# Optimization experiments

Measured on AMD Instinct MI355X. Metric: run time of the kernel, lower is better.

Reference implementation:

```python
import jax, jax.numpy as jnp
import numpy as np


def _elu(x):
    return jnp.where(x > 0, x, jnp.expm1(x))


def setup_inputs() -> dict:
    key = jax.random.key(0)
    ks = jax.random.split(key, 12)
    B, T, E, A, S, H, L = 1024, 50, 1024, 6, 200, 200, 30
    g = lambda k, shape, s=0.05: (jax.random.normal(k, shape, jnp.float32) * s)
    return {
        "action": jax.random.normal(ks[0], (B, T, A), jnp.float32),
        "embed": jax.random.normal(ks[1], (B, T, E), jnp.float32),
        "noise": jax.random.normal(ks[2], (B, T, L), jnp.float32),
        # GRUCell params (PyTorch gate order r,z,n), stored as [in, 3S]
        "W_ih": g(ks[3], (A + E, 3 * S)),
        "W_hh": g(ks[4], (S, 3 * S)),
        "b_ih": jnp.zeros((3 * S,), jnp.float32),
        "b_hh": jnp.zeros((3 * S,), jnp.float32),
        # fc_prior: Linear(S,H) -> ELU -> Linear(H, 2L)
        "Wp1": g(ks[5], (S, H)), "bp1": jnp.zeros((H,), jnp.float32),
        "Wp2": g(ks[6], (H, 2 * L)), "bp2": jnp.zeros((2 * L,), jnp.float32),
        # fc_posterior: Linear(S+E,H) -> ELU -> Linear(H, 2L)
        "Wq1": g(ks[7], (S + E, H)), "bq1": jnp.zeros((H,), jnp.float32),
        "Wq2": g(ks[8], (H, 2 * L)), "bq2": jnp.zeros((2 * L,), jnp.float32),
    }


def reference(action, embed, noise, W_ih, W_hh, b_ih, b_hh,
              Wp1, bp1, Wp2, bp2, Wq1, bq1, Wq2, bq2):
    B = action.shape[0]
    S = W_hh.shape[0]

    def gru(x, h):
        # PyTorch GRUCell: gates r, z, n
        gi = x @ W_ih + b_ih
        gh = h @ W_hh + b_hh
        i_r, i_z, i_n = jnp.split(gi, 3, -1)
        h_r, h_z, h_n = jnp.split(gh, 3, -1)
        r = jax.nn.sigmoid(i_r + h_r)
        z = jax.nn.sigmoid(i_z + h_z)
        n = jnp.tanh(i_n + r * h_n)
        return (1.0 - z) * n + z * h

    def step(deter, inp):
        a_t, e_t, eps_t = inp  # [B,A], [B,E], [B,L]
        deter = gru(jnp.concatenate([a_t, e_t], -1), deter)
        pm, ps = jnp.split(_elu(deter @ Wp1 + bp1) @ Wp2 + bp2, 2, -1)
        qm, qs = jnp.split(
            _elu(jnp.concatenate([deter, e_t], -1) @ Wq1 + bq1) @ Wq2 + bq2, 2, -1)
        ps = jax.nn.softplus(ps) + 0.1
        qs = jax.nn.softplus(qs) + 0.1
        stoch = qm + qs * eps_t  # posterior rsample
        return deter, (deter, stoch, pm, ps, qm, qs)

    deter0 = jnp.zeros((B, S), action.dtype)
    xs = (jnp.swapaxes(action, 0, 1),
          jnp.swapaxes(embed, 0, 1),
          jnp.swapaxes(noise, 0, 1))
    _, outs = jax.lax.scan(step, deter0, xs)
    # [T,B,*] -> [B,T,*]; pack (deter, stoch, prior mean/std, post mean/std)
    outs = [jnp.swapaxes(o, 0, 1) for o in outs]
    return jnp.concatenate(outs, -1)  # [B, T, S + 5L]
```

## Files before the change

### kernel.cpp

```cpp
#include <hip/hip_runtime.h>
#include <hip/hip_bf16.h>
#include <cstdint>


typedef __attribute__((ext_vector_type(8))) short   short8;
typedef __attribute__((ext_vector_type(8))) __bf16  bf16x8;
typedef __attribute__((ext_vector_type(4))) float   f32x4;

__device__ __forceinline__ float bf2f(unsigned short u) {
    unsigned int v = ((unsigned int)u) << 16;
    return __builtin_bit_cast(float, v);
}
__device__ __forceinline__ unsigned short f2bf(float f) {
    unsigned int v = __builtin_bit_cast(unsigned int, f);
    v = v + 0x7FFFu + ((v >> 16) & 1u);
    return (unsigned short)(v >> 16);
}
__device__ __forceinline__ float softplusf(float x) {
    return (x > 20.f) ? x : log1pf(__expf(x));
}
__device__ __forceinline__ void gload_lds16(const void* g, void* l) {
    __builtin_amdgcn_global_load_lds(
        (const __attribute__((address_space(1))) void*)g,
        (__attribute__((address_space(3))) void*)l, 16, 0, 0);
}

#define OFF_BPACK 81920000
#define OFF_WHH   83558400
#define OFF_WPQ1  83837952
#define OFF_WPQ2  84024320


__global__ __launch_bounds__(256) void pack_kernel(
    const float* __restrict__ W_ih, const float* __restrict__ W_hh,
    const float* __restrict__ Wp1,  const float* __restrict__ Wq1,
    const float* __restrict__ Wp2,  const float* __restrict__ Wq2,
    unsigned short* __restrict__ Bpack, unsigned short* __restrict__ Whh_p,
    unsigned short* __restrict__ Wpq1,  unsigned short* __restrict__ Wpq2)
{
    int e = blockIdx.x * 256 + threadIdx.x;
    if (e < 819200) {
        const int j = e & 7, l = (e >> 3) & 63;
        const int nt = (e >> 9) % 50, kk = e / (512 * 50);
        const int k = kk * 32 + (l >> 4) * 8 + j;
        const int c = nt * 16 + (l & 15);
        Bpack[e] = f2bf((c < 600) ? W_ih[(6 + k) * 600 + c]
                                  : Wq1[(200 + k) * 200 + (c - 600)]);
        return;
    }
    e -= 819200;
    if (e < 139776) {
        const int j = e & 7, l = (e >> 3) & 63;
        const int nt = (e >> 9) % 39, kk = e / (512 * 39);
        const int k = kk * 32 + (l >> 4) * 8 + j;
        const int g = nt / 13, st = nt % 13;
        const int c = st * 16 + (l & 15);
        Whh_p[e] = (k < 200 && c < 200) ? f2bf(W_hh[k * 600 + g * 200 + c]) : (unsigned short)0;
        return;
    }
    e -= 139776;
    if (e < 93184) {
        const int j = e & 7, l = (e >> 3) & 63;
        const int nt = (e >> 9) % 26, kk = e / (512 * 26);
        const int k = kk * 32 + (l >> 4) * 8 + j;
        unsigned short v = 0;
        if (nt < 13) { const int c = nt * 16 + (l & 15);        if (k < 200 && c < 200) v = f2bf(Wp1[k * 200 + c]); }
        else         { const int c = (nt - 13) * 16 + (l & 15); if (k < 200 && c < 200) v = f2bf(Wq1[k * 200 + c]); }
        Wpq1[e] = v;
        return;
    }
    e -= 93184;
    if (e < 28672) {
        const int j = e & 7, l = (e >> 3) & 63;
        const int nt = (e >> 9) % 8, kk = e / (512 * 8);
        const int k = kk * 32 + (l >> 4) * 8 + j;
        unsigned short v = 0;
        if (nt < 4) { const int c = nt * 16 + (l & 15);       if (k < 200 && c < 60) v = f2bf(Wp2[k * 60 + c]); }
        else        { const int c = (nt - 4) * 16 + (l & 15); if (k < 200 && c < 60) v = f2bf(Wq2[k * 60 + c]); }
        Wpq2[e] = v;
    }
}

#define K1_BYTES 26624
__global__ __launch_bounds__(256, 3) void k1_gi(
    const float* __restrict__ embed,
    const float* __restrict__ action,
    const float* __restrict__ W_ih,
    const float* __restrict__ b_ih,
    const float* __restrict__ bq1,
    const unsigned short* __restrict__ Bpack,
    unsigned short* __restrict__ GI)
{
    __shared__ char bufS[2][K1_BYTES];

    const int tid = threadIdx.x;
    const int w = tid >> 6, l = tid & 63;
    const int lo = l & 15, hi = l >> 4;

    const int g    = (blockIdx.x & 7) * 250 + (blockIdx.x >> 3);
    const int mblk = g / 5;
    const int ng   = g - mblk * 5;
    const int rb   = mblk * 128;

    const char* sp[7]; int st[7]; int dof[7];
    const int nch = (w < 2) ? 7 : 6;
#pragma unroll
    for (int i = 0; i < 7; ++i) {
        int j = w + 4 * i; if (j >= 26) j = 25;
        if (j < 10) {
            sp[i]  = (const char*)Bpack + (size_t)(ng * 10 + j) * 1024 + l * 16;
            st[i]  = 50 * 1024;
            dof[i] = j * 1024;
        } else {
            const int a = j - 10;
            sp[i]  = (const char*)embed
                   + (size_t)(rb + a * 8 + (l >> 3)) * 4096 + (l & 7) * 16;
            st[i]  = 128;
            dof[i] = 10240 + a * 1024;
        }
    }

    f32x4 acc[2][10];
#pragma unroll
    for (int m = 0; m < 2; ++m)
#pragma unroll
        for (int i = 0; i < 10; ++i) acc[m][i] = f32x4{0.f, 0.f, 0.f, 0.f};

#pragma unroll
    for (int i = 0; i < 7; ++i) if (i < nch) {
        gload_lds16(sp[i], &bufS[0][dof[i]]);
        sp[i] += st[i];
    }

    int cur = 0;
    for (int kk = 0; kk < 32; ++kk) {
        const int nxt = cur ^ 1;
        if (kk < 31) {
#pragma unroll
            for (int i = 0; i < 7; ++i) if (i < nch) {
                gload_lds16(sp[i], &bufS[nxt][dof[i]]);
                sp[i] += st[i];
            }
            if (w < 2) asm volatile("s_waitcnt vmcnt(7)" ::: "memory");
            else       asm volatile("s_waitcnt vmcnt(6)" ::: "memory");
        } else {
            asm volatile("s_waitcnt vmcnt(0)" ::: "memory");
        }
        __builtin_amdgcn_s_barrier();
        __builtin_amdgcn_sched_barrier(0);

        const float* Af = (const float*)&bufS[cur][10240];
        bf16x8 af[2];
#pragma unroll
        for (int m = 0; m < 2; ++m) {
            const int ms = w * 2 + m;
            const float* rp = Af + (ms * 16 + lo) * 32 + hi * 8;
            f32x4 v0 = *(const f32x4*)rp;
            f32x4 v1 = *(const f32x4*)(rp + 4);
            bf16x8 t;
#pragma unroll
            for (int q = 0; q < 4; ++q) { t[q] = (__bf16)v0[q]; t[4 + q] = (__bf16)v1[q]; }
            af[m] = t;
        }
#pragma unroll
        for (int i = 0; i < 10; ++i) {
            bf16x8 b = __builtin_bit_cast(bf16x8,
                *(const short8*)&bufS[cur][i * 1024 + l * 16]);
            acc[0][i] = __builtin_amdgcn_mfma_f32_16x16x32_bf16(af[0], b, acc[0][i], 0, 0, 0);
            acc[1][i] = __builtin_amdgcn_mfma_f32_16x16x32_bf16(af[1], b, acc[1][i], 0, 0, 0);
        }

        asm volatile("s_waitcnt lgkmcnt(0)" ::: "memory");
        __builtin_amdgcn_s_barrier();
        __builtin_amdgcn_sched_barrier(0);
        cur = nxt;
    }

#pragma unroll
    for (int m = 0; m < 2; ++m) {
        const int rbase = rb + (w * 2 + m) * 16 + hi * 4;
        float av[4][6];
#pragma unroll
        for (int r = 0; r < 4; ++r)
#pragma unroll
            for (int k = 0; k < 6; ++k) av[r][k] = action[(size_t)(rbase + r) * 6 + k];
#pragma unroll
        for (int i = 0; i < 10; ++i) {
            const int col = ng * 160 + i * 16 + lo;
            const float bias = (col < 600) ? b_ih[col] : bq1[col - 600];
            float wa[6];
            if (col < 600) {
#pragma unroll
                for (int k = 0; k < 6; ++k) wa[k] = W_ih[k * 600 + col];
            }
#pragma unroll
            for (int r = 0; r < 4; ++r) {
                float v = acc[m][i][r] + bias;
                if (col < 600) {
#pragma unroll
                    for (int k = 0; k < 6; ++k) v += av[r][k] * wa[k];
                }
                GI[(size_t)(rbase + r) * 800 + col] = f2bf(v);
            }
        }
    }
}

#define HSTRB 232
#define GSTR  227

__global__ __launch_bounds__(512, 2) void k2_scan(
    unsigned short* __restrict__ GI,
    const unsigned short* __restrict__ Whh_p,
    const float* __restrict__ b_hh,
    float* __restrict__ out)
{
    __shared__ unsigned short hS[16 * HSTRB];
    __shared__ float gAll[3 * 16 * GSTR];
    __shared__ __align__(16) unsigned short GIbuf[2][12288];

    const int tid = threadIdx.x;
    const int w = tid >> 6, l = tid & 63;
    const int lo = l & 15, hi = l >> 4;
    const int r0 = blockIdx.x * 16;

    for (int i = tid; i < 16 * HSTRB; i += 512) hS[i] = 0;

    const int t0 = w * 5;
    const int ntl = (w == 7) ? 4 : 5;
    bf16x8 wf[5][7];
#pragma unroll
    for (int i = 0; i < 5; ++i)
#pragma unroll
        for (int kk = 0; kk < 7; ++kk)
            if (i < ntl)
                wf[i][kk] = __builtin_bit_cast(bf16x8,
                    *(const short8*)&Whh_p[((kk * 39 + (t0 + i)) * 64 + l) * 8]);

    int gOff[5];
#pragma unroll
    for (int i = 0; i < 5; ++i) {
        int nt = t0 + i; if (nt > 38) nt = 38;
        const int g = nt / 13, st = nt - g * 13;
        gOff[i] = (g * 16 + hi * 4) * GSTR + st * 16 + lo;
    }

    const char* srcB[3];
#pragma unroll
    for (int i = 0; i < 3; ++i) {
        int j = (i * 8 + w) * 64 + l;
        int rj = j / 75; int cj = j - rj * 75;
        if (rj > 15) { rj = 15; cj = 74; }
        srcB[i] = (const char*)GI + (size_t)(r0 + rj) * 50 * 1600 + (size_t)cj * 16;
    }

    const int c = tid & 255;
    const int rh = tid >> 8;
    const bool act = (c < 200);
    float bh0 = 0.f, bh1 = 0.f, bh2 = 0.f;
    if (act) { bh0 = b_hh[c]; bh1 = b_hh[200 + c]; bh2 = b_hh[400 + c]; }
    float h_reg[8] = {0.f, 0.f, 0.f, 0.f, 0.f, 0.f, 0.f, 0.f};

    {
#pragma unroll
        for (int i = 0; i < 3; ++i)
            gload_lds16(srcB[i], &GIbuf[0][(i * 8 + w) * 512]);
    }
    asm volatile("s_waitcnt lgkmcnt(0)" ::: "memory");
    __builtin_amdgcn_s_barrier();
    __builtin_amdgcn_sched_barrier(0);

    for (int t = 0; t < 50; ++t) {
        const int tn = (t < 49) ? t + 1 : 49;
        const int bsel = (t + 1) & 1;
#pragma unroll
        for (int i = 0; i < 3; ++i)
            gload_lds16(srcB[i] + (size_t)tn * 1600, &GIbuf[bsel][(i * 8 + w) * 512]);

        bf16x8 hf[7];
#pragma unroll
        for (int kk = 0; kk < 7; ++kk)
            hf[kk] = __builtin_bit_cast(bf16x8,
                *(const short8*)&hS[lo * HSTRB + kk * 32 + hi * 8]);
        f32x4 acc[5];
#pragma unroll
        for (int i = 0; i < 5; ++i) acc[i] = f32x4{0.f, 0.f, 0.f, 0.f};
#pragma unroll
        for (int i = 0; i < 5; ++i) if (i < ntl)
#pragma unroll
            for (int kk = 0; kk < 7; ++kk)
                acc[i] = __builtin_amdgcn_mfma_f32_16x16x32_bf16(hf[kk], wf[i][kk], acc[i], 0, 0, 0);

#pragma unroll
        for (int i = 0; i < 5; ++i) if (i < ntl)
#pragma unroll
            for (int r = 0; r < 4; ++r)
                gAll[gOff[i] + r * GSTR] = acc[i][r];

        asm volatile("s_waitcnt lgkmcnt(0)" ::: "memory");
        __builtin_amdgcn_s_barrier();
        __builtin_amdgcn_sched_barrier(0);
        asm volatile("s_waitcnt vmcnt(3)" ::: "memory");
        __builtin_amdgcn_sched_barrier(0);

        if (act) {
            const unsigned short* gib = &GIbuf[t & 1][0];
#pragma unroll
            for (int rr = 0; rr < 8; ++rr) {
                const int row = rh * 8 + rr;
                const float gi_r = bf2f(gib[row * 600 + c]);
                const float gi_z = bf2f(gib[row * 600 + 200 + c]);
                const float gi_n = bf2f(gib[row * 600 + 400 + c]);
                const float gr = gi_r + gAll[(0 * 16 + row) * GSTR + c] + bh0;
                const float gz = gi_z + gAll[(1 * 16 + row) * GSTR + c] + bh1;
                const float hn = gAll[(2 * 16 + row) * GSTR + c] + bh2;
                const float rs = __builtin_amdgcn_rcpf(1.f + __expf(-gr));
                const float zz = __builtin_amdgcn_rcpf(1.f + __expf(-gz));
                const float x  = gi_n + rs * hn;
                const float e2 = __expf(-2.f * fabsf(x));
                float th = (1.f - e2) * __builtin_amdgcn_rcpf(1.f + e2);
                th = __builtin_copysignf(th, x);
                const float h = (1.f - zz) * th + zz * h_reg[rr];
                h_reg[rr] = h;
                hS[row * HSTRB + c] = f2bf(h);
                const size_t bt = (size_t)((r0 + row) * 50 + t);
                out[bt * 350 + c] = h;
                GI[bt * 800 + c]  = f2bf(h);
            }
        }

        asm volatile("s_waitcnt lgkmcnt(0)" ::: "memory");
        __builtin_amdgcn_s_barrier();
        __builtin_amdgcn_sched_barrier(0);
    }
}

__global__ __launch_bounds__(256, 1) void k3_heads(
    const unsigned short* __restrict__ GI,
    const unsigned short* __restrict__ Wpq1,
    const unsigned short* __restrict__ Wpq2,
    const float* __restrict__ noise,
    const float* __restrict__ bp1,
    const float* __restrict__ bp2,
    const float* __restrict__ bq2,
    float* __restrict__ out)
{
    __shared__ unsigned short pq[2][16 * HSTRB];
    __shared__ float ost[16 * 128];

    const int tid = threadIdx.x;
    const int w = tid >> 6, l = tid & 63;
    const int lo = l & 15, hi = l >> 4;
    const int r0 = blockIdx.x * 16;

    {   unsigned short* p0 = &pq[0][0];
        for (int i = tid; i < 2 * 16 * HSTRB; i += 256) p0[i] = 0; }
    __syncthreads();

    bf16x8 af[7];
#pragma unroll
    for (int kk = 0; kk < 7; ++kk)
        af[kk] = __builtin_bit_cast(bf16x8,
            *(const short8*)&GI[(size_t)(r0 + lo) * 800 + kk * 32 + hi * 8]);

    const int h1s = (w < 2) ? 7 * w : 14 + 6 * (w - 2);
    const int h1n = (w < 2) ? 7 : 6;
    f32x4 a2[7];
#pragma unroll
    for (int i = 0; i < 7; ++i) a2[i] = f32x4{0.f, 0.f, 0.f, 0.f};
#pragma unroll
    for (int i = 0; i < 7; ++i) if (i < h1n) {
        const int nt = h1s + i;
#pragma unroll
        for (int kk = 0; kk < 7; ++kk) {
            bf16x8 b = __builtin_bit_cast(bf16x8,
                *(const short8*)&Wpq1[((kk * 26 + nt) * 64 + l) * 8]);
            a2[i] = __builtin_amdgcn_mfma_f32_16x16x32_bf16(af[kk], b, a2[i], 0, 0, 0);
        }
    }
#pragma unroll
    for (int i = 0; i < 7; ++i) if (i < h1n) {
        const int nt = h1s + i;
        const bool isq = (nt >= 13);
        const int c1 = (isq ? (nt - 13) : nt) * 16 + lo;
        if (c1 < 200) {
#pragma unroll
            for (int r = 0; r < 4; ++r) {
                const int row = hi * 4 + r;
                float v = a2[i][r];
                if (isq) v += bf2f(GI[(size_t)(r0 + row) * 800 + 600 + c1]);
                else     v += bp1[c1];
                v = (v > 0.f) ? v : expm1f(v);
                pq[isq ? 1 : 0][row * HSTRB + c1] = f2bf(v);
            }
        }
    }
    __syncthreads();

    const unsigned short* srcS = &pq[(w >= 2) ? 1 : 0][0];
    bf16x8 pf[7];
#pragma unroll
    for (int kk = 0; kk < 7; ++kk)
        pf[kk] = __builtin_bit_cast(bf16x8,
            *(const short8*)&srcS[lo * HSTRB + kk * 32 + hi * 8]);
    f32x4 a3[2];
    a3[0] = f32x4{0.f, 0.f, 0.f, 0.f};
    a3[1] = f32x4{0.f, 0.f, 0.f, 0.f};
#pragma unroll
    for (int i = 0; i < 2; ++i) {
        const int nt = ((w >= 2) ? 4 : 0) + (w & 1) * 2 + i;
#pragma unroll
        for (int kk = 0; kk < 7; ++kk) {
            bf16x8 b = __builtin_bit_cast(bf16x8,
                *(const short8*)&Wpq2[((kk * 8 + nt) * 64 + l) * 8]);
            a3[i] = __builtin_amdgcn_mfma_f32_16x16x32_bf16(pf[kk], b, a3[i], 0, 0, 0);
        }
    }
#pragma unroll
    for (int i = 0; i < 2; ++i) {
        const int nt = ((w >= 2) ? 4 : 0) + (w & 1) * 2 + i;
        const int cl = (nt & 3) * 16 + lo;
        if (cl < 60) {
            const float bb = (nt < 4) ? bp2[cl] : bq2[cl];
            const int obase = ((nt < 4) ? 0 : 64) + ((cl < 30) ? cl : (32 + cl - 30));
#pragma unroll
            for (int r = 0; r < 4; ++r)
                ost[(hi * 4 + r) * 128 + obase] = a3[i][r] + bb;
        }
    }
    __syncthreads();

    for (int idx = tid; idx < 16 * 150; idx += 256) {
        const int row = idx / 150;
        const int c = 200 + (idx - row * 150);
        const size_t bt = (size_t)(r0 + row);
        const float* o = &ost[row * 128];
        float v;
        if (c < 230) {
            const int j = c - 200;
            const float qs = softplusf(o[96 + j]) + 0.1f;
            v = o[64 + j] + qs * noise[bt * 30 + j];
        }
        else if (c < 260) v = o[c - 230];
        else if (c < 290) v = softplusf(o[32 + (c - 260)]) + 0.1f;
        else if (c < 320) v = o[64 + (c - 290)];
        else              v = softplusf(o[96 + (c - 320)]) + 0.1f;
        out[bt * 350 + c] = v;
    }
}

extern "C" void kernel_launch(void* const* d_in, const int* in_sizes, int n_in,
                              void* d_out, int out_size, void* d_ws, size_t ws_size,
                              hipStream_t stream)
{
    const float* action = (const float*)d_in[0];
    const float* embed  = (const float*)d_in[1];
    const float* noise  = (const float*)d_in[2];
    const float* W_ih   = (const float*)d_in[3];
    const float* W_hh   = (const float*)d_in[4];
    const float* b_ih   = (const float*)d_in[5];
    const float* b_hh   = (const float*)d_in[6];
    const float* Wp1    = (const float*)d_in[7];
    const float* bp1    = (const float*)d_in[8];
    const float* Wp2    = (const float*)d_in[9];
    const float* bp2    = (const float*)d_in[10];
    const float* Wq1    = (const float*)d_in[11];
    const float* bq1    = (const float*)d_in[12];
    const float* Wq2    = (const float*)d_in[13];
    const float* bq2    = (const float*)d_in[14];
    (void)in_sizes; (void)n_in; (void)out_size; (void)ws_size;

    char* ws = (char*)d_ws;
    unsigned short* GI    = (unsigned short*)(ws);
    unsigned short* Bpack = (unsigned short*)(ws + OFF_BPACK);
    unsigned short* Whh_p = (unsigned short*)(ws + OFF_WHH);
    unsigned short* Wpq1  = (unsigned short*)(ws + OFF_WPQ1);
    unsigned short* Wpq2  = (unsigned short*)(ws + OFF_WPQ2);
    float* outp = (float*)d_out;

    pack_kernel<<<4222, 256, 0, stream>>>(W_ih, W_hh, Wp1, Wq1, Wp2, Wq2,
                                          Bpack, Whh_p, Wpq1, Wpq2);
    k1_gi<<<2000, 256, 0, stream>>>(embed, action, W_ih, b_ih, bq1, Bpack, GI);
    k2_scan<<<64, 512, 0, stream>>>(GI, Whh_p, b_hh, outp);
    k3_heads<<<3200, 256, 0, stream>>>(GI, Wpq1, Wpq2, noise, bp1, bp2, bq2, outp);
}
```

Before: 369.8 us.

## Stage bf16-converted embed tiles in LDS and retile k1 warps as 2x2

The GI GEMM kernel now loads embed rows into registers, converts them to bf16 once, and writes them to LDS. Before, fp32 rows were copied straight into LDS and every warp converted them again. This halves the A-tile footprint in LDS and removes redundant conversions. Warps are rearranged from a 1x4 row split with 10 column tiles each to a 2x2 grid with 4 row by 5 column MFMA tiles, which improves operand reuse per LDS read. In exchange, launch bounds drop from 3 to 2 blocks per CU, and the register-staged prefetch adds extra vmcnt and barrier ordering.

```diff
diff --git a/kernel.cpp b/kernel.cpp
--- a/kernel.cpp
+++ b/kernel.cpp
@@ -81,8 +81,9 @@
     }
 }
 
-#define K1_BYTES 26624
-__global__ __launch_bounds__(256, 3) void k1_gi(
+#define K1_BYTES 18432
+#define K1_AOFF  10240
+__global__ __launch_bounds__(256, 2) void k1_gi(
     const float* __restrict__ embed,
     const float* __restrict__ action,
     const float* __restrict__ W_ih,
@@ -96,50 +97,79 @@
     const int tid = threadIdx.x;
     const int w = tid >> 6, l = tid & 63;
     const int lo = l & 15, hi = l >> 4;
+    const int mq = w >> 1;
+    const int nq = w & 1;
 
     const int g    = (blockIdx.x & 7) * 250 + (blockIdx.x >> 3);
     const int mblk = g / 5;
     const int ng   = g - mblk * 5;
     const int rb   = mblk * 128;
 
-    const char* sp[7]; int st[7]; int dof[7];
-    const int nch = (w < 2) ? 7 : 6;
-#pragma unroll
-    for (int i = 0; i < 7; ++i) {
-        int j = w + 4 * i; if (j >= 26) j = 25;
-        if (j < 10) {
-            sp[i]  = (const char*)Bpack + (size_t)(ng * 10 + j) * 1024 + l * 16;
-            st[i]  = 50 * 1024;
-            dof[i] = j * 1024;
-        } else {
-            const int a = j - 10;
-            sp[i]  = (const char*)embed
-                   + (size_t)(rb + a * 8 + (l >> 3)) * 4096 + (l & 7) * 16;
-            st[i]  = 128;
-            dof[i] = 10240 + a * 1024;
-        }
-    }
-
-    f32x4 acc[2][10];
-#pragma unroll
-    for (int m = 0; m < 2; ++m)
-#pragma unroll
-        for (int i = 0; i < 10; ++i) acc[m][i] = f32x4{0.f, 0.f, 0.f, 0.f};
-
-#pragma unroll
-    for (int i = 0; i < 7; ++i) if (i < nch) {
-        gload_lds16(sp[i], &bufS[0][dof[i]]);
-        sp[i] += st[i];
-    }
+    const char* bsp[3]; int bdof[3];
+    const int nB = (w < 2) ? 3 : 2;
+#pragma unroll
+    for (int i = 0; i < 3; ++i) {
+        int j = w + 4 * i; if (j >= 10) j = 9;
+        bsp[i]  = (const char*)Bpack + (size_t)(ng * 10 + j) * 1024 + l * 16;
+        bdof[i] = j * 1024;
+    }
+
+    const int msA = tid >> 6;
+    const int lA  = tid & 63;
+    const float* aSrc1 = embed + (size_t)(rb + msA * 16 + (lA & 15)) * 1024 + (lA >> 4) * 8;
+    const float* aSrc2 = aSrc1 + (size_t)64 * 1024;
+    const int awo1 = K1_AOFF + msA * 1024 + lA * 16;
+    const int awo2 = awo1 + 4096;
+
+    f32x4 acc[4][5];
+#pragma unroll
+    for (int s = 0; s < 4; ++s)
+#pragma unroll
+        for (int i = 0; i < 5; ++i) acc[s][i] = f32x4{0.f, 0.f, 0.f, 0.f};
+
+    {
+        f32x4 a1a = *(const f32x4*)(aSrc1);
+        f32x4 a1b = *(const f32x4*)(aSrc1 + 4);
+        f32x4 a2a = *(const f32x4*)(aSrc2);
+        f32x4 a2b = *(const f32x4*)(aSrc2 + 4);
+        __builtin_amdgcn_sched_barrier(0);
+#pragma unroll
+        for (int i = 0; i < 3; ++i) if (i < nB) {
+            gload_lds16(bsp[i], &bufS[0][bdof[i]]);
+            bsp[i] += 51200;
+        }
+        if (w < 2) asm volatile("s_waitcnt vmcnt(3)" ::: "memory");
+        else       asm volatile("s_waitcnt vmcnt(2)" ::: "memory");
+        __builtin_amdgcn_sched_barrier(0);
+        bf16x8 t1, t2;
+#pragma unroll
+        for (int q = 0; q < 4; ++q) {
+            t1[q] = (__bf16)a1a[q]; t1[4 + q] = (__bf16)a1b[q];
+            t2[q] = (__bf16)a2a[q]; t2[4 + q] = (__bf16)a2b[q];
+        }
+        *(short8*)&bufS[0][awo1] = __builtin_bit_cast(short8, t1);
+        *(short8*)&bufS[0][awo2] = __builtin_bit_cast(short8, t2);
+    }
+    asm volatile("s_waitcnt lgkmcnt(0)" ::: "memory");
+    __builtin_amdgcn_s_barrier();
+    __builtin_amdgcn_sched_barrier(0);
 
     int cur = 0;
     for (int kk = 0; kk < 32; ++kk) {
         const int nxt = cur ^ 1;
+        f32x4 a1a, a1b, a2a, a2b;
         if (kk < 31) {
-#pragma unroll
-            for (int i = 0; i < 7; ++i) if (i < nch) {
-                gload_lds16(sp[i], &bufS[nxt][dof[i]]);
-                sp[i] += st[i];
+            const float* p1 = aSrc1 + (size_t)(kk + 1) * 32;
+            const float* p2 = aSrc2 + (size_t)(kk + 1) * 32;
+            a1a = *(const f32x4*)(p1);
+            a1b = *(const f32x4*)(p1 + 4);
+            a2a = *(const f32x4*)(p2);
+            a2b = *(const f32x4*)(p2 + 4);
+            __builtin_amdgcn_sched_barrier(0);
+#pragma unroll
+            for (int i = 0; i < 3; ++i) if (i < nB) {
+                gload_lds16(bsp[i], &bufS[nxt][bdof[i]]);
+                bsp[i] += 51200;
             }
             if (w < 2) asm volatile("s_waitcnt vmcnt(7)" ::: "memory");
             else       asm volatile("s_waitcnt vmcnt(6)" ::: "memory");
@@ -149,25 +179,32 @@
         __builtin_amdgcn_s_barrier();
         __builtin_amdgcn_sched_barrier(0);
 
-        const float* Af = (const float*)&bufS[cur][10240];
-        bf16x8 af[2];
-#pragma unroll
-        for (int m = 0; m < 2; ++m) {
-            const int ms = w * 2 + m;
-            const float* rp = Af + (ms * 16 + lo) * 32 + hi * 8;
-            f32x4 v0 = *(const f32x4*)rp;
-            f32x4 v1 = *(const f32x4*)(rp + 4);
-            bf16x8 t;
-#pragma unroll
-            for (int q = 0; q < 4; ++q) { t[q] = (__bf16)v0[q]; t[4 + q] = (__bf16)v1[q]; }
-            af[m] = t;
-        }
-#pragma unroll
-        for (int i = 0; i < 10; ++i) {
+        bf16x8 af[4];
+#pragma unroll
+        for (int s = 0; s < 4; ++s)
+            af[s] = __builtin_bit_cast(bf16x8,
+                *(const short8*)&bufS[cur][K1_AOFF + (mq * 4 + s) * 1024 + l * 16]);
+#pragma unroll
+        for (int i = 0; i < 5; ++i) {
             bf16x8 b = __builtin_bit_cast(bf16x8,
-                *(const short8*)&bufS[cur][i * 1024 + l * 16]);
-            acc[0][i] = __builtin_amdgcn_mfma_f32_16x16x32_bf16(af[0], b, acc[0][i], 0, 0, 0);
-            acc[1][i] = __builtin_amdgcn_mfma_f32_16x16x32_bf16(af[1], b, acc[1][i], 0, 0, 0);
+                *(const short8*)&bufS[cur][(nq * 5 + i) * 1024 + l * 16]);
+#pragma unroll
+            for (int s = 0; s < 4; ++s)
+                acc[s][i] = __builtin_amdgcn_mfma_f32_16x16x32_bf16(af[s], b, acc[s][i], 0, 0, 0);
+        }
+
+        if (kk < 31) {
+            if (w < 2) asm volatile("s_waitcnt vmcnt(3)" ::: "memory");
+            else       asm volatile("s_waitcnt vmcnt(2)" ::: "memory");
+            __builtin_amdgcn_sched_barrier(0);
+            bf16x8 t1, t2;
+#pragma unroll
+            for (int q = 0; q < 4; ++q) {
+                t1[q] = (__bf16)a1a[q]; t1[4 + q] = (__bf16)a1b[q];
+                t2[q] = (__bf16)a2a[q]; t2[4 + q] = (__bf16)a2b[q];
+            }
+            *(short8*)&bufS[nxt][awo1] = __builtin_bit_cast(short8, t1);
+            *(short8*)&bufS[nxt][awo2] = __builtin_bit_cast(short8, t2);
         }
 
         asm volatile("s_waitcnt lgkmcnt(0)" ::: "memory");
@@ -177,16 +214,16 @@
     }
 
 #pragma unroll
-    for (int m = 0; m < 2; ++m) {
-        const int rbase = rb + (w * 2 + m) * 16 + hi * 4;
+    for (int s = 0; s < 4; ++s) {
+        const int rbase = rb + (mq * 4 + s) * 16 + hi * 4;
         float av[4][6];
 #pragma unroll
         for (int r = 0; r < 4; ++r)
 #pragma unroll
             for (int k = 0; k < 6; ++k) av[r][k] = action[(size_t)(rbase + r) * 6 + k];
 #pragma unroll
-        for (int i = 0; i < 10; ++i) {
-            const int col = ng * 160 + i * 16 + lo;
+        for (int i = 0; i < 5; ++i) {
+            const int col = ng * 160 + (nq * 5 + i) * 16 + lo;
             const float bias = (col < 600) ? b_ih[col] : bq1[col - 600];
             float wa[6];
             if (col < 600) {
@@ -195,7 +232,7 @@
             }
 #pragma unroll
             for (int r = 0; r < 4; ++r) {
-                float v = acc[m][i][r] + bias;
+                float v = acc[s][i][r] + bias;
                 if (col < 600) {
 #pragma unroll
                     for (int k = 0; k < 6; ++k) v += av[r][k] * wa[k];
```

After: 423.9 us. 1.15x slower.

## Retile input-projection GEMM to 1024-thread blocks and double k3 row tile

Applied to the files above, without the earlier changes.

k1_gi now runs 1024-thread blocks, each covering 128 rows and 400 columns (two column groups instead of five). Embed is loaded through registers and converted to bf16 once before going into LDS, so each wave no longer converts fp32 A tiles itself. The goal is to cut how often A tiles are reloaded across column groups and to shrink the A traffic in LDS. k3_heads now handles 32 rows per block, so each weight fragment is reused across two MFMA row groups, at the cost of more registers and LDS per block.

```diff
diff --git a/kernel.cpp b/kernel.cpp
--- a/kernel.cpp
+++ b/kernel.cpp
@@ -81,8 +81,9 @@
     }
 }
 
-#define K1_BYTES 26624
-__global__ __launch_bounds__(256, 3) void k1_gi(
+#define K1_BYTES 33792
+#define K1_AOFF  25600
+__global__ __launch_bounds__(1024, 4) void k1_gi(
     const float* __restrict__ embed,
     const float* __restrict__ action,
     const float* __restrict__ W_ih,
@@ -97,77 +98,95 @@
     const int w = tid >> 6, l = tid & 63;
     const int lo = l & 15, hi = l >> 4;
 
-    const int g    = (blockIdx.x & 7) * 250 + (blockIdx.x >> 3);
-    const int mblk = g / 5;
-    const int ng   = g - mblk * 5;
+    const int gsw  = (blockIdx.x & 7) * 100 + (blockIdx.x >> 3);
+    const int mblk = gsw >> 1;
+    const int ng   = gsw & 1;
     const int rb   = mblk * 128;
 
-    const char* sp[7]; int st[7]; int dof[7];
-    const int nch = (w < 2) ? 7 : 6;
-#pragma unroll
-    for (int i = 0; i < 7; ++i) {
-        int j = w + 4 * i; if (j >= 26) j = 25;
-        if (j < 10) {
-            sp[i]  = (const char*)Bpack + (size_t)(ng * 10 + j) * 1024 + l * 16;
-            st[i]  = 50 * 1024;
-            dof[i] = j * 1024;
-        } else {
-            const int a = j - 10;
-            sp[i]  = (const char*)embed
-                   + (size_t)(rb + a * 8 + (l >> 3)) * 4096 + (l & 7) * 16;
-            st[i]  = 128;
-            dof[i] = 10240 + a * 1024;
-        }
-    }
-
-    f32x4 acc[2][10];
-#pragma unroll
-    for (int m = 0; m < 2; ++m)
-#pragma unroll
-        for (int i = 0; i < 10; ++i) acc[m][i] = f32x4{0.f, 0.f, 0.f, 0.f};
-
-#pragma unroll
-    for (int i = 0; i < 7; ++i) if (i < nch) {
-        gload_lds16(sp[i], &bufS[0][dof[i]]);
-        sp[i] += st[i];
-    }
+    const char* bsp[2]; int bdof[2];
+    const int nB = (w < 9) ? 2 : 1;
+#pragma unroll
+    for (int i = 0; i < 2; ++i) {
+        int j = w + 16 * i; if (j >= 25) j = 24;
+        bsp[i]  = (const char*)Bpack + (size_t)(ng * 25 + j) * 1024 + l * 16;
+        bdof[i] = j * 1024;
+    }
+
+    const int ms  = tid >> 7;
+    const int la  = (tid & 127) >> 1;
+    const int hf2 = tid & 1;
+    const float* aSrc = embed + (size_t)(rb + ms * 16 + (la & 15)) * 1024
+                      + (la >> 4) * 8 + hf2 * 4;
+    const int awo = K1_AOFF + ms * 1024 + la * 16 + hf2 * 8;
+
+    const int msw = w >> 1;
+    const int nq  = w & 1;
+    const int nn  = nq ? 12 : 13;
+    const int tb  = nq * 13;
+
+    f32x4 acc[13];
+#pragma unroll
+    for (int i = 0; i < 13; ++i) acc[i] = f32x4{0.f, 0.f, 0.f, 0.f};
+
+    {
+        f32x4 a0 = *(const f32x4*)aSrc;
+        __builtin_amdgcn_sched_barrier(0);
+#pragma unroll
+        for (int i = 0; i < 2; ++i) if (i < nB) {
+            gload_lds16(bsp[i], &bufS[0][bdof[i]]);
+            bsp[i] += 51200;
+        }
+        if (w < 9) asm volatile("s_waitcnt vmcnt(2)" ::: "memory");
+        else       asm volatile("s_waitcnt vmcnt(1)" ::: "memory");
+        __builtin_amdgcn_sched_barrier(0);
+        unsigned long long v =
+              (unsigned long long)f2bf(a0[0])
+            | ((unsigned long long)f2bf(a0[1]) << 16)
+            | ((unsigned long long)f2bf(a0[2]) << 32)
+            | ((unsigned long long)f2bf(a0[3]) << 48);
+        *(unsigned long long*)&bufS[0][awo] = v;
+    }
+    asm volatile("s_waitcnt lgkmcnt(0)" ::: "memory");
 
     int cur = 0;
     for (int kk = 0; kk < 32; ++kk) {
         const int nxt = cur ^ 1;
+        f32x4 a1;
         if (kk < 31) {
-#pragma unroll
-            for (int i = 0; i < 7; ++i) if (i < nch) {
-                gload_lds16(sp[i], &bufS[nxt][dof[i]]);
-                sp[i] += st[i];
+            a1 = *(const f32x4*)(aSrc + (size_t)(kk + 1) * 32);
+            __builtin_amdgcn_sched_barrier(0);
+#pragma unroll
+            for (int i = 0; i < 2; ++i) if (i < nB) {
+                gload_lds16(bsp[i], &bufS[nxt][bdof[i]]);
+                bsp[i] += 51200;
             }
-            if (w < 2) asm volatile("s_waitcnt vmcnt(7)" ::: "memory");
-            else       asm volatile("s_waitcnt vmcnt(6)" ::: "memory");
+            if (w < 9) asm volatile("s_waitcnt vmcnt(3)" ::: "memory");
+            else       asm volatile("s_waitcnt vmcnt(2)" ::: "memory");
         } else {
             asm volatile("s_waitcnt vmcnt(0)" ::: "memory");
         }
         __builtin_amdgcn_s_barrier();
         __builtin_amdgcn_sched_barrier(0);
 
-        const float* Af = (const float*)&bufS[cur][10240];
-        bf16x8 af[2];
-#pragma unroll
-        for (int m = 0; m < 2; ++m) {
-            const int ms = w * 2 + m;
-            const float* rp = Af + (ms * 16 + lo) * 32 + hi * 8;
-            f32x4 v0 = *(const f32x4*)rp;
-            f32x4 v1 = *(const f32x4*)(rp + 4);
-            bf16x8 t;
-#pragma unroll
-            for (int q = 0; q < 4; ++q) { t[q] = (__bf16)v0[q]; t[4 + q] = (__bf16)v1[q]; }
-            af[m] = t;
-        }
-#pragma unroll
-        for (int i = 0; i < 10; ++i) {
+        bf16x8 af = __builtin_bit_cast(bf16x8,
+            *(const short8*)&bufS[cur][K1_AOFF + msw * 1024 + l * 16]);
+#pragma unroll
+        for (int i = 0; i < 13; ++i) if (i < nn) {
             bf16x8 b = __builtin_bit_cast(bf16x8,
-                *(const short8*)&bufS[cur][i * 1024 + l * 16]);
-            acc[0][i] = __builtin_amdgcn_mfma_f32_16x16x32_bf16(af[0], b, acc[0][i], 0, 0, 0);
-            acc[1][i] = __builtin_amdgcn_mfma_f32_16x16x32_bf16(af[1], b, acc[1][i], 0, 0, 0);
+                *(const short8*)&bufS[cur][(tb + i) * 1024 + l * 16]);
+            acc[i] = __builtin_amdgcn_mfma_f32_16x16x32_bf16(af, b, acc[i], 0, 0, 0);
+        }
+
+        if (kk < 31) {
+            if (w < 9) asm volatile("s_waitcnt vmcnt(2)" ::: "memory");
+            else       asm volatile("s_waitcnt vmcnt(1)" ::: "memory");
+            __builtin_amdgcn_sched_barrier(0);
+            unsigned long long v =
+                  (unsigned long long)f2bf(a1[0])
+                | ((unsigned long long)f2bf(a1[1]) << 16)
+                | ((unsigned long long)f2bf(a1[2]) << 32)
+                | ((unsigned long long)f2bf(a1[3]) << 48);
+            *(unsigned long long*)&bufS[nxt][awo] = v;
         }
 
         asm volatile("s_waitcnt lgkmcnt(0)" ::: "memory");
@@ -176,17 +195,16 @@
         cur = nxt;
     }
 
-#pragma unroll
-    for (int m = 0; m < 2; ++m) {
-        const int rbase = rb + (w * 2 + m) * 16 + hi * 4;
+    {
+        const int rbase = rb + msw * 16 + hi * 4;
         float av[4][6];
 #pragma unroll
         for (int r = 0; r < 4; ++r)
 #pragma unroll
             for (int k = 0; k < 6; ++k) av[r][k] = action[(size_t)(rbase + r) * 6 + k];
 #pragma unroll
-        for (int i = 0; i < 10; ++i) {
-            const int col = ng * 160 + i * 16 + lo;
+        for (int i = 0; i < 13; ++i) if (i < nn) {
+            const int col = ng * 400 + (tb + i) * 16 + lo;
             const float bias = (col < 600) ? b_ih[col] : bq1[col - 600];
             float wa[6];
             if (col < 600) {
@@ -195,7 +213,7 @@
             }
 #pragma unroll
             for (int r = 0; r < 4; ++r) {
-                float v = acc[m][i][r] + bias;
+                float v = acc[i][r] + bias;
                 if (col < 600) {
 #pragma unroll
                     for (int k = 0; k < 6; ++k) v += av[r][k] * wa[k];
@@ -345,29 +363,33 @@
     const float* __restrict__ bq2,
     float* __restrict__ out)
 {
-    __shared__ unsigned short pq[2][16 * HSTRB];
-    __shared__ float ost[16 * 128];
+    __shared__ unsigned short pq[2][32 * HSTRB];
+    __shared__ float ost[32 * 128];
 
     const int tid = threadIdx.x;
     const int w = tid >> 6, l = tid & 63;
     const int lo = l & 15, hi = l >> 4;
-    const int r0 = blockIdx.x * 16;
+    const int r0 = blockIdx.x * 32;
 
     {   unsigned short* p0 = &pq[0][0];
-        for (int i = tid; i < 2 * 16 * HSTRB; i += 256) p0[i] = 0; }
+        for (int i = tid; i < 2 * 32 * HSTRB; i += 256) p0[i] = 0; }
     __syncthreads();
 
-    bf16x8 af[7];
-#pragma unroll
-    for (int kk = 0; kk < 7; ++kk)
-        af[kk] = __builtin_bit_cast(bf16x8,
-            *(const short8*)&GI[(size_t)(r0 + lo) * 800 + kk * 32 + hi * 8]);
+    bf16x8 af[2][7];
+#pragma unroll
+    for (int rg = 0; rg < 2; ++rg)
+#pragma unroll
+        for (int kk = 0; kk < 7; ++kk)
+            af[rg][kk] = __builtin_bit_cast(bf16x8,
+                *(const short8*)&GI[(size_t)(r0 + rg * 16 + lo) * 800 + kk * 32 + hi * 8]);
 
     const int h1s = (w < 2) ? 7 * w : 14 + 6 * (w - 2);
     const int h1n = (w < 2) ? 7 : 6;
-    f32x4 a2[7];
-#pragma unroll
-    for (int i = 0; i < 7; ++i) a2[i] = f32x4{0.f, 0.f, 0.f, 0.f};
+    f32x4 a2[2][7];
+#pragma unroll
+    for (int rg = 0; rg < 2; ++rg)
+#pragma unroll
+        for (int i = 0; i < 7; ++i) a2[rg][i] = f32x4{0.f, 0.f, 0.f, 0.f};
 #pragma unroll
     for (int i = 0; i < 7; ++i) if (i < h1n) {
         const int nt = h1s + i;
@@ -375,7 +397,8 @@
         for (int kk = 0; kk < 7; ++kk) {
             bf16x8 b = __builtin_bit_cast(bf16x8,
                 *(const short8*)&Wpq1[((kk * 26 + nt) * 64 + l) * 8]);
-            a2[i] = __builtin_amdgcn_mfma_f32_16x16x32_bf16(af[kk], b, a2[i], 0, 0, 0);
+            a2[0][i] = __builtin_amdgcn_mfma_f32_16x16x32_bf16(af[0][kk], b, a2[0][i], 0, 0, 0);
+            a2[1][i] = __builtin_amdgcn_mfma_f32_16x16x32_bf16(af[1][kk], b, a2[1][i], 0, 0, 0);
         }
     }
 #pragma unroll
@@ -385,27 +408,34 @@
         const int c1 = (isq ? (nt - 13) : nt) * 16 + lo;
         if (c1 < 200) {
 #pragma unroll
-            for (int r = 0; r < 4; ++r) {
-                const int row = hi * 4 + r;
-                float v = a2[i][r];
-                if (isq) v += bf2f(GI[(size_t)(r0 + row) * 800 + 600 + c1]);
-                else     v += bp1[c1];
-                v = (v > 0.f) ? v : expm1f(v);
-                pq[isq ? 1 : 0][row * HSTRB + c1] = f2bf(v);
-            }
+            for (int rg = 0; rg < 2; ++rg)
+#pragma unroll
+                for (int r = 0; r < 4; ++r) {
+                    const int lrow = rg * 16 + hi * 4 + r;
+                    float v = a2[rg][i][r];
+                    if (isq) v += bf2f(GI[(size_t)(r0 + lrow) * 800 + 600 + c1]);
+                    else     v += bp1[c1];
+                    v = (v > 0.f) ? v : expm1f(v);
+                    pq[isq ? 1 : 0][lrow * HSTRB + c1] = f2bf(v);
+                }
         }
     }
     __syncthreads();
 
     const unsigned short* srcS = &pq[(w >= 2) ? 1 : 0][0];
-    bf16x8 pf[7];
-#pragma unroll
-    for (int kk = 0; kk < 7; ++kk)
-        pf[kk] = __builtin_bit_cast(bf16x8,
-            *(const short8*)&srcS[lo * HSTRB + kk * 32 + hi * 8]);
-    f32x4 a3[2];
-    a3[0] = f32x4{0.f, 0.f, 0.f, 0.f};
-    a3[1] = f32x4{0.f, 0.f, 0.f, 0.f};
+    bf16x8 pf[2][7];
+#pragma unroll
+    for (int rg = 0; rg < 2; ++rg)
+#pragma unroll
+        for (int kk = 0; kk < 7; ++kk)
+            pf[rg][kk] = __builtin_bit_cast(bf16x8,
+                *(const short8*)&srcS[(rg * 16 + lo) * HSTRB + kk * 32 + hi * 8]);
+    f32x4 a3[2][2];
+#pragma unroll
+    for (int rg = 0; rg < 2; ++rg) {
+        a3[rg][0] = f32x4{0.f, 0.f, 0.f, 0.f};
+        a3[rg][1] = f32x4{0.f, 0.f, 0.f, 0.f};
+    }
 #pragma unroll
     for (int i = 0; i < 2; ++i) {
         const int nt = ((w >= 2) ? 4 : 0) + (w & 1) * 2 + i;
@@ -413,7 +443,8 @@
         for (int kk = 0; kk < 7; ++kk) {
             bf16x8 b = __builtin_bit_cast(bf16x8,
                 *(const short8*)&Wpq2[((kk * 8 + nt) * 64 + l) * 8]);
-            a3[i] = __builtin_amdgcn_mfma_f32_16x16x32_bf16(pf[kk], b, a3[i], 0, 0, 0);
+            a3[0][i] = __builtin_amdgcn_mfma_f32_16x16x32_bf16(pf[0][kk], b, a3[0][i], 0, 0, 0);
+            a3[1][i] = __builtin_amdgcn_mfma_f32_16x16x32_bf16(pf[1][kk], b, a3[1][i], 0, 0, 0);
         }
     }
 #pragma unroll
@@ -424,13 +455,15 @@
             const float bb = (nt < 4) ? bp2[cl] : bq2[cl];
             const int obase = ((nt < 4) ? 0 : 64) + ((cl < 30) ? cl : (32 + cl - 30));
 #pragma unroll
-            for (int r = 0; r < 4; ++r)
-                ost[(hi * 4 + r) * 128 + obase] = a3[i][r] + bb;
+            for (int rg = 0; rg < 2; ++rg)
+#pragma unroll
+                for (int r = 0; r < 4; ++r)
+                    ost[(rg * 16 + hi * 4 + r) * 128 + obase] = a3[rg][i][r] + bb;
         }
     }
     __syncthreads();
 
-    for (int idx = tid; idx < 16 * 150; idx += 256) {
+    for (int idx = tid; idx < 32 * 150; idx += 256) {
         const int row = idx / 150;
         const int c = 200 + (idx - row * 150);
         const size_t bt = (size_t)(r0 + row);
@@ -480,7 +513,7 @@
 
     pack_kernel<<<4222, 256, 0, stream>>>(W_ih, W_hh, Wp1, Wq1, Wp2, Wq2,
                                           Bpack, Whh_p, Wpq1, Wpq2);
-    k1_gi<<<2000, 256, 0, stream>>>(embed, action, W_ih, b_ih, bq1, Bpack, GI);
+    k1_gi<<<800, 1024, 0, stream>>>(embed, action, W_ih, b_ih, bq1, Bpack, GI);
     k2_scan<<<64, 512, 0, stream>>>(GI, Whh_p, b_hh, outp);
-    k3_heads<<<3200, 256, 0, stream>>>(GI, Wpq1, Wpq2, noise, bp1, bp2, bq2, outp);
-}
+    k3_heads<<<1600, 256, 0, stream>>>(GI, Wpq1, Wpq2, noise, bp1, bp2, bq2, outp);
+}
```

Result: slower. 435.9 us (+17.9%).
